# Optimization experiments

Measured on AMD Instinct MI355X. Metric: run time of the kernel, lower is better.

Reference implementation:

```python
import jax, jax.numpy as jnp
import numpy as np

N_NODES = 100_000
N_EDGES = 1_600_000
VOCAB = 128
NUM_GRAPHS = 2048


def setup_inputs() -> dict:
    key = jax.random.key(0)
    ks = jax.random.split(key, 8)
    node_ids = jax.random.randint(ks[0], (N_NODES,), 0, VOCAB)
    edge_index = jax.random.randint(ks[1], (2, N_EDGES), 0, N_NODES)
    batch = jnp.sort(jax.random.randint(ks[2], (N_NODES,), 0, NUM_GRAPHS))
    emb = jax.random.normal(ks[3], (VOCAB, 64), jnp.float32) * 0.1
    W1 = jax.random.normal(ks[4], (64, 128), jnp.float32) * (1.0 / np.sqrt(64))
    b1 = jnp.zeros((128,), jnp.float32)
    W2 = jax.random.normal(ks[5], (128, 64), jnp.float32) * (1.0 / np.sqrt(128))
    b2 = jnp.zeros((64,), jnp.float32)
    fc_w = jax.random.normal(ks[6], (1, 64), jnp.float32) * (1.0 / np.sqrt(64))
    fc_b = jnp.zeros((1,), jnp.float32)
    return {"node_ids": node_ids, "edge_index": edge_index, "batch": batch,
            "emb": emb, "W1": W1, "b1": b1, "W2": W2, "b2": b2,
            "fc_w": fc_w, "fc_b": fc_b}


def _gcn_layer(x, W, b, src, dst, norm, n_nodes):
    # x: [N, Fin] -> transform then gather-normalize-scatter (PyG GCNConv)
    h = x @ W                                   # [N, Fout]
    msg = norm[:, None] * h[src]                # [E+N, Fout]
    out = jax.ops.segment_sum(msg, dst, num_segments=n_nodes)
    return out + b


def reference(node_ids, edge_index, batch, emb, W1, b1, W2, b2, fc_w, fc_b):
    n = node_ids.shape[0]
    loop = jnp.arange(n, dtype=edge_index.dtype)
    src = jnp.concatenate([edge_index[0], loop])    # self-loops added (GCNConv default)
    dst = jnp.concatenate([edge_index[1], loop])
    # symmetric normalization: deg^{-1/2}[src] * deg^{-1/2}[dst], deg from dst (in-degree incl. self-loop)
    deg = jax.ops.segment_sum(jnp.ones_like(src, dtype=jnp.float32), dst, num_segments=n)
    dis = jax.lax.rsqrt(jnp.maximum(deg, 1.0))
    norm = dis[src] * dis[dst]

    x = emb[node_ids]                                # [N, 64]
    x = jax.nn.relu(_gcn_layer(x, W1, b1, src, dst, norm, n))
    x = jax.nn.relu(_gcn_layer(x, W2, b2, src, dst, norm, n))

    # global mean pool over graphs
    counts = jax.ops.segment_sum(jnp.ones((n,), jnp.float32), batch, num_segments=NUM_GRAPHS)
    pooled = jax.ops.segment_sum(x, batch, num_segments=NUM_GRAPHS)
    pooled = pooled / jnp.maximum(counts, 1.0)[:, None]   # [G, 64]
    # dropout is identity in eval mode
    logits = pooled @ fc_w.T + fc_b                 # [G, 1]
    return jax.nn.sigmoid(logits).squeeze(-1)       # [G]
```

## Files before the change

kernel.cpp:

```cpp
#include <hip/hip_runtime.h>
#include <math.h>

typedef short short8 __attribute__((ext_vector_type(8)));
typedef float f32x4 __attribute__((ext_vector_type(4)));

#define WP 132
#define OP 136
#define SC_C 8192
#define SC_NB 832
#define GCAP 1024
#define DG_SUB 16
#define DG_LCAP 1024


__device__ __forceinline__ short f2bf(float x) {
    unsigned u = __float_as_uint(x);
    u += 0x7fffu + ((u >> 16) & 1u);
    return (short)(u >> 16);
}

__global__ void k_cnt(const int* __restrict__ dst, int* __restrict__ wcnt,
                      int E, int N) {
    int lane = threadIdx.x & 63;
    int gw = blockIdx.x * 4 + (threadIdx.x >> 6);
    int TOT = gridDim.x * 4;
    int cnt[8] = {0, 0, 0, 0, 0, 0, 0, 0};
    for (long long base = (long long)gw * 64; base < E; base += (long long)TOT * 64) {
        int i = (int)base + lane;
        bool valid = (i < E);
        int d = valid ? dst[i] : 0;
        int b = valid ? (int)(((long long)d * 8) / N) : -1;
#pragma unroll
        for (int k = 0; k < 8; ++k)
            cnt[k] += (int)__popcll(__ballot(b == k));
    }
#pragma unroll
    for (int k = 0; k < 8; ++k)
        if (lane == 0) wcnt[k * TOT + gw] = cnt[k];
}

__global__ void k_scat(const int* __restrict__ src, const int* __restrict__ dst,
                       const int* __restrict__ wscan, unsigned* __restrict__ sp1,
                       int E, int N) {
    int lane = threadIdx.x & 63;
    int gw = blockIdx.x * 4 + (threadIdx.x >> 6);
    int TOT = gridDim.x * 4;
    int cur[8];
#pragma unroll
    for (int k = 0; k < 8; ++k) cur[k] = wscan[k * TOT + gw];
    for (long long base = (long long)gw * 64; base < E; base += (long long)TOT * 64) {
        int i = (int)base + lane;
        bool valid = (i < E);
        int d = 0, s = 0;
        if (valid) { d = dst[i]; s = src[i]; }
        int b = valid ? (int)(((long long)d * 8) / N) : -1;
        unsigned packed = 0;
        if (valid) {
            int lo = (int)((long long)N * b / 8);
            packed = ((unsigned)s << 14) | (unsigned)(d - lo);
        }
#pragma unroll
        for (int k = 0; k < 8; ++k) {
            unsigned long long mk = __ballot(b == k);
            if (b == k) {
                int pref = (int)__popcll(mk & ((1ull << lane) - 1ull));
                sp1[cur[k] + pref] = packed;
            }
            cur[k] += (int)__popcll(mk);
        }
    }
}

__global__ __launch_bounds__(1024) void k_deg3(
        const unsigned* __restrict__ sp1, const int* __restrict__ wscan,
        int* __restrict__ degi2, int E, int N, int TOTW) {
    __shared__ int h[DG_LCAP];
    int b   = blockIdx.x & 7;
    int hf  = (blockIdx.x >> 3) & 1;
    int sb  = blockIdx.x >> 4;
    int tid = threadIdx.x;
    int lo = (int)((long long)N * b / 8);
    int hi = (int)((long long)N * (b + 1) / 8);
    int range = hi - lo;
    int sub = (range + DG_SUB - 1) / DG_SUB;
    int nlo = sb * sub;
    int nhi = min(nlo + sub, range);
    int cnt = nhi - nlo;
    if (cnt <= 0) return;
    for (int i = tid; i < cnt; i += 1024) h[i] = 0;
    __syncthreads();
    int beg = wscan[b * TOTW];
    int end = (b < 7) ? wscan[(b + 1) * TOTW] : E;
    int span = end - beg;
    int hb = beg + hf * (span >> 1);
    int he = (hf == 0) ? (beg + (span >> 1)) : end;
    for (int i = hb + tid; i < he; i += 1024) {
        int dl = (int)(sp1[i] & 16383u) - nlo;
        if ((unsigned)dl < (unsigned)cnt) atomicAdd(&h[dl], 1);
    }
    __syncthreads();
    int* dout = degi2 + (size_t)hf * N + lo + nlo;
    for (int i = tid; i < cnt; i += 1024) dout[i] = h[i];
}

__global__ void k_tcur(const int* __restrict__ rowptr, int* __restrict__ tcur,
                       int T, int N) {
    int t = blockIdx.x * 256 + threadIdx.x;
    if (t < T) tcur[t] = rowptr[min(16 * t, N)];
}

__global__ __launch_bounds__(256) void k_scat2(
        const unsigned* __restrict__ sp1, const int* __restrict__ wscan,
        int* __restrict__ tcur, unsigned* __restrict__ sp2,
        int E, int N, int TOTW) {
    __shared__ unsigned staged[SC_C];
    __shared__ int hist[SC_NB], hstart[SC_NB], hoff[SC_NB], gbase[SC_NB];
    __shared__ int sdata[256];
    int b = blockIdx.x & 7;
    int nb = gridDim.x >> 3, bi = blockIdx.x >> 3;
    int lo = (int)((long long)N * b / 8);
    int t0 = lo >> 4;
    int beg = wscan[b * TOTW];
    int end = (b < 7) ? wscan[(b + 1) * TOTW] : E;
    int tid = threadIdx.x;

    for (int cb = beg + bi * SC_C; cb < end; cb += nb * SC_C) {
        int count = min(SC_C, end - cb);
        for (int j = tid; j < SC_NB; j += 256) hist[j] = 0;
        __syncthreads();

        unsigned v[SC_C / 256];
#pragma unroll
        for (int j = 0; j < SC_C / 256; ++j) {
            int i = j * 256 + tid;
            v[j] = 0;
            if (i < count) {
                unsigned sp = sp1[cb + i];
                v[j] = sp;
                int d = (int)(sp & 16383u) + lo;
                atomicAdd(&hist[(d >> 4) - t0], 1);
            }
        }
        __syncthreads();

        int loc[4]; int lsum = 0;
#pragma unroll
        for (int j = 0; j < 4; ++j) {
            int idx = tid * 4 + j;
            loc[j] = (idx < SC_NB) ? hist[idx] : 0;
            lsum += loc[j];
        }
        sdata[tid] = lsum;
        __syncthreads();
        for (int off = 1; off < 256; off <<= 1) {
            int add = (tid >= off) ? sdata[tid - off] : 0;
            __syncthreads();
            sdata[tid] += add;
            __syncthreads();
        }
        int excl = sdata[tid] - lsum;
        int run = 0;
#pragma unroll
        for (int j = 0; j < 4; ++j) {
            int idx = tid * 4 + j;
            if (idx < SC_NB) { hstart[idx] = excl + run; hoff[idx] = excl + run; }
            run += loc[j];
        }
        __syncthreads();

        for (int j = tid; j < SC_NB; j += 256)
            if (hist[j] > 0) gbase[j] = atomicAdd(&tcur[t0 + j], hist[j]);
#pragma unroll
        for (int j = 0; j < SC_C / 256; ++j) {
            int i = j * 256 + tid;
            if (i < count) {
                int d = (int)(v[j] & 16383u) + lo;
                int bin = (d >> 4) - t0;
                int old = atomicAdd(&hoff[bin], 1);
                staged[old] = v[j];
            }
        }
        __syncthreads();

        for (int i = tid; i < count; i += 256) {
            unsigned sp = staged[i];
            int d = (int)(sp & 16383u) + lo;
            int bin = (d >> 4) - t0;
            int pos = gbase[bin] + (i - hstart[bin]);
            unsigned s = sp >> 14;
            sp2[pos] = (s << 4) | (unsigned)(d & 15);
        }
        __syncthreads();
    }
}

__global__ void k_scan_a(const int* __restrict__ in, const int* __restrict__ in2,
                         int* __restrict__ outp, int* __restrict__ csums,
                         float* __restrict__ dis, const int* __restrict__ nid,
                         int2* __restrict__ ndpk, int n) {
    __shared__ int sdata[256];
    int tid = threadIdx.x;
    int idx = blockIdx.x * 1024 + tid * 4;
    int v[4];
#pragma unroll
    for (int j = 0; j < 4; ++j) {
        v[j] = 0;
        if (idx + j < n) {
            v[j] = in[idx + j];
            if (in2 != nullptr) v[j] += in2[idx + j];
            if (dis != nullptr) {
                float dv = rsqrtf((float)(v[j] + 1));
                dis[idx + j] = dv;
                int2 nd; nd.x = nid[idx + j]; nd.y = __float_as_int(dv);
                ndpk[idx + j] = nd;
            }
        }
    }
    int tsum = v[0] + v[1] + v[2] + v[3];
    sdata[tid] = tsum;
    __syncthreads();
    for (int off = 1; off < 256; off <<= 1) {
        int add = (tid >= off) ? sdata[tid - off] : 0;
        __syncthreads();
        sdata[tid] += add;
        __syncthreads();
    }
    int excl = sdata[tid] - tsum;
    int run = 0;
#pragma unroll
    for (int j = 0; j < 4; ++j) {
        if (idx + j < n) outp[idx + j] = excl + run;
        run += v[j];
    }
    if (tid == 255) csums[blockIdx.x] = sdata[255];
}

__global__ void k_scan_b(int* __restrict__ csums, int nch) {
    __shared__ int sdata[256];
    int tid = threadIdx.x;
    int v[4];
#pragma unroll
    for (int j = 0; j < 4; ++j) {
        int i = tid * 4 + j;
        v[j] = (i < nch) ? csums[i] : 0;
    }
    int tsum = v[0] + v[1] + v[2] + v[3];
    sdata[tid] = tsum;
    __syncthreads();
    for (int off = 1; off < 256; off <<= 1) {
        int add = (tid >= off) ? sdata[tid - off] : 0;
        __syncthreads();
        sdata[tid] += add;
        __syncthreads();
    }
    int excl = sdata[tid] - tsum;
    int run = 0;
#pragma unroll
    for (int j = 0; j < 4; ++j) {
        int i = tid * 4 + j;
        if (i < nch) csums[i] = excl + run;
        run += v[j];
    }
}

__global__ void k_scan_c(int* __restrict__ outp, const int* __restrict__ csums,
                         int n, int E, int writeTail) {
    int idx = blockIdx.x * 1024 + threadIdx.x * 4;
    int add = csums[blockIdx.x];
#pragma unroll
    for (int j = 0; j < 4; ++j)
        if (idx + j < n) outp[idx + j] += add;
    if (writeTail && blockIdx.x == 0 && threadIdx.x == 0) outp[n] = E;
}

__global__ void k_tabs(const float* __restrict__ emb, const float* __restrict__ W1,
                       const float* __restrict__ W2,
                       short* __restrict__ T1T, short* __restrict__ W2T) {
    int id = blockIdx.x * 256 + threadIdx.x;
    if (id < 128 * 128) {
        int f = id >> 7, c = id & 127;
        float acc = 0.f;
#pragma unroll
        for (int k = 0; k < 64; ++k) acc += emb[c * 64 + k] * W1[k * 128 + f];
        T1T[id] = f2bf(acc);
    } else {
        int id2 = id - 128 * 128;
        if (id2 < 64 * 128) {
            int f = id2 >> 7, k = id2 & 127;
            W2T[id2] = f2bf(W2[k * 64 + f]);
        }
    }
}

__global__ __launch_bounds__(256) void k_fused(
        const int* __restrict__ rowptr, const unsigned* __restrict__ sp2,
        const int2* __restrict__ ndpk, const float* __restrict__ dis,
        const short* __restrict__ T1T, const short* __restrict__ W2T,
        const float* __restrict__ b1, unsigned short* __restrict__ g, int N) {
    __shared__ float wtile[16 * WP];
    __shared__ unsigned short otile[16 * OP];
    int tid = threadIdx.x;
    int v0 = blockIdx.x * 16;
    int nloc = min(16, N - v0);

    for (int i = tid; i < 16 * WP; i += 256) wtile[i] = 0.f;
    __syncthreads();

    if (tid < nloc) {
        int2 nd = ndpk[v0 + tid];
        atomicAdd(&wtile[tid * WP + nd.x], __int_as_float(nd.y));
    }
    int e0 = rowptr[v0], e1 = rowptr[min(v0 + 16, N)];
    for (int base = e0; base < e1; base += 1024) {
        unsigned sp[4];
        int2 nd[4];
#pragma unroll
        for (int j = 0; j < 4; ++j) {
            int i = base + tid + j * 256;
            sp[j] = (i < e1) ? sp2[i] : 0xffffffffu;
        }
#pragma unroll
        for (int j = 0; j < 4; ++j)
            if (sp[j] != 0xffffffffu) nd[j] = ndpk[sp[j] >> 4];
#pragma unroll
        for (int j = 0; j < 4; ++j)
            if (sp[j] != 0xffffffffu)
                atomicAdd(&wtile[(sp[j] & 15u) * WP + nd[j].x],
                          __int_as_float(nd[j].y));
    }
    __syncthreads();

    int wid = tid >> 6, lane = tid & 63;
    int m = lane & 15, g4 = lane >> 4;

    short8 a[4];
#pragma unroll
    for (int s = 0; s < 4; ++s) {
        float av[8];
        *(f32x4*)(av)     = *(const f32x4*)&wtile[m * WP + g4 * 8 + s * 32];
        *(f32x4*)(av + 4) = *(const f32x4*)&wtile[m * WP + g4 * 8 + s * 32 + 4];
        short8 f;
#pragma unroll
        for (int i = 0; i < 8; ++i) f[i] = f2bf(av[i]);
        a[s] = f;
    }
    float dvals[4];
#pragma unroll
    for (int r = 0; r < 4; ++r) {
        int v = v0 + g4 * 4 + r;
        dvals[r] = (v < N) ? dis[v] : 0.f;
    }

#pragma unroll
    for (int t = 0; t < 2; ++t) {
        int nt = wid * 2 + t;
        f32x4 acc = {0.f, 0.f, 0.f, 0.f};
        const short8* bp = (const short8*)(T1T + (size_t)(nt * 16 + m) * 128 + g4 * 8);
#pragma unroll
        for (int s = 0; s < 4; ++s)
            acc = __builtin_amdgcn_mfma_f32_16x16x32_bf16(a[s], bp[s * 4], acc, 0, 0, 0);
        int col = nt * 16 + m;
        float bb = b1[col];
#pragma unroll
        for (int r = 0; r < 4; ++r) {
            int row = g4 * 4 + r;
            otile[row * OP + col] =
                (unsigned short)f2bf(fmaxf(dvals[r] * acc[r] + bb, 0.f));
        }
    }
    __syncthreads();

    short8 a2[4];
#pragma unroll
    for (int s = 0; s < 4; ++s)
        a2[s] = *(const short8*)&otile[m * OP + g4 * 8 + s * 32];
    {
        int nt2 = wid;
        f32x4 acc = {0.f, 0.f, 0.f, 0.f};
        const short8* bp = (const short8*)(W2T + (size_t)(nt2 * 16 + m) * 128 + g4 * 8);
#pragma unroll
        for (int s = 0; s < 4; ++s)
            acc = __builtin_amdgcn_mfma_f32_16x16x32_bf16(a2[s], bp[s * 4], acc, 0, 0, 0);
#pragma unroll
        for (int r = 0; r < 4; ++r) {
            int row = g4 * 4 + r;
            if (row < nloc)
                g[(size_t)(v0 + row) * 64 + nt2 * 16 + m] =
                    (unsigned short)f2bf(dvals[r] * acc[r]);
        }
    }
}

__global__ __launch_bounds__(256) void k_gather3(
        const unsigned* __restrict__ sp2, const int* __restrict__ rowptr,
        const unsigned short* __restrict__ g, const float* __restrict__ dis,
        const float* __restrict__ b2, float* __restrict__ x, int N) {
    __shared__ int lbuf[GCAP];
    __shared__ int lrp[17];
    __shared__ int ncur[16];
    int tid = threadIdx.x;
    int v0 = blockIdx.x * 16;
    int nloc = min(16, N - v0);
    if (tid < 17) lrp[tid] = rowptr[min(v0 + tid, N)];
    __syncthreads();
    int e0 = lrp[0], e1 = lrp[nloc];
    int span = e1 - e0;
    bool fits = (span <= GCAP);

    if (fits) {
        if (tid < 16) ncur[tid] = lrp[tid] - e0;
        __syncthreads();
        for (int i = e0 + tid; i < e1; i += 256) {
            unsigned sp = sp2[i];
            int old = atomicAdd(&ncur[sp & 15u], 1);
            lbuf[old] = (int)(sp >> 4);
        }
        __syncthreads();
    }

    int q = tid >> 4, l = tid & 15;
    if (q >= nloc) return;
    int v = v0 + q;
    const uint2* g64 = (const uint2*)g;

    uint2 su = g64[(size_t)v * 16 + l];
    f32x4 acc;
    acc[0] = __uint_as_float(su.x << 16);
    acc[1] = __uint_as_float(su.x & 0xffff0000u);
    acc[2] = __uint_as_float(su.y << 16);
    acc[3] = __uint_as_float(su.y & 0xffff0000u);

    if (fits) {
        int e = lrp[q] - e0, re = lrp[q + 1] - e0;
        while (e < re) {
            int cnt = re - e;
            uint2 u[8];
#pragma unroll
            for (int j = 0; j < 8; ++j) {
                int s = lbuf[min(e + j, re - 1)];
                u[j] = g64[(size_t)s * 16 + l];
            }
#pragma unroll
            for (int j = 0; j < 8; ++j) {
                float mask = (j < cnt) ? 1.f : 0.f;
                acc[0] += mask * __uint_as_float(u[j].x << 16);
                acc[1] += mask * __uint_as_float(u[j].x & 0xffff0000u);
                acc[2] += mask * __uint_as_float(u[j].y << 16);
                acc[3] += mask * __uint_as_float(u[j].y & 0xffff0000u);
            }
            e += 8;
        }
    } else {
        for (int i = e0; i < e1; ++i) {
            unsigned sp = sp2[i];
            if ((int)(sp & 15u) == q) {
                int s = (int)(sp >> 4);
                uint2 u = g64[(size_t)s * 16 + l];
                acc[0] += __uint_as_float(u.x << 16);
                acc[1] += __uint_as_float(u.x & 0xffff0000u);
                acc[2] += __uint_as_float(u.y << 16);
                acc[3] += __uint_as_float(u.y & 0xffff0000u);
            }
        }
    }
    float dv = dis[v];
    f32x4 bb = *(const f32x4*)(b2 + l * 4);
    f32x4 r;
#pragma unroll
    for (int j = 0; j < 4; ++j) r[j] = fmaxf(dv * acc[j] + bb[j], 0.f);
    *(f32x4*)(x + (size_t)v * 64 + l * 4) = r;
}

__global__ void k_bounds(const int* __restrict__ batch, int* __restrict__ gstart,
                         int* __restrict__ gend, int n) {
    int i = blockIdx.x * 256 + threadIdx.x;
    if (i >= n) return;
    int b = batch[i];
    if (i == 0 || batch[i - 1] != b) gstart[b] = i;
    if (i == n - 1 || batch[i + 1] != b) gend[b] = i + 1;
}

__global__ __launch_bounds__(256) void k_pool2(
        const float* __restrict__ x, const int* __restrict__ gstart,
        const int* __restrict__ gend, const float* __restrict__ fc_w,
        const float* __restrict__ fc_b, float* __restrict__ out) {
    __shared__ float red[4][64];
    int gi = blockIdx.x;
    int tid = threadIdx.x, wid = tid >> 6, lane = tid & 63;
    int s = gstart[gi], epos = gend[gi];
    float acc = 0.f;
    for (int r = s + wid; r < epos; r += 4) acc += x[(size_t)r * 64 + lane];
    red[wid][lane] = acc;
    __syncthreads();
    if (wid == 0) {
        float a = red[0][lane] + red[1][lane] + red[2][lane] + red[3][lane];
        float cnt = fmaxf((float)(epos - s), 1.0f);
        a = (a / cnt) * fc_w[lane];
#pragma unroll
        for (int off = 32; off >= 1; off >>= 1) a += __shfl_down(a, off);
        if (lane == 0) out[gi] = 1.0f / (1.0f + expf(-(a + fc_b[0])));
    }
}

extern "C" void kernel_launch(void* const* d_in, const int* in_sizes, int n_in,
                              void* d_out, int out_size, void* d_ws, size_t ws_size,
                              hipStream_t stream) {
    const int*   nid   = (const int*)d_in[0];
    const int*   eidx  = (const int*)d_in[1];
    const int*   batch = (const int*)d_in[2];
    const float* emb   = (const float*)d_in[3];
    const float* W1    = (const float*)d_in[4];
    const float* b1    = (const float*)d_in[5];
    const float* W2    = (const float*)d_in[6];
    const float* b2    = (const float*)d_in[7];
    const float* fcw   = (const float*)d_in[8];
    const float* fcb   = (const float*)d_in[9];

    const int N = in_sizes[0];
    const int E = in_sizes[1] / 2;
    const int G = out_size;
    const int T = (N + 15) / 16;
    const int* src = eidx;
    const int* dst = eidx + E;

    char* p = (char*)d_ws;
    auto alloc = [&](size_t bytes) {
        char* r = p;
        p += (bytes + 255) & ~(size_t)255;
        return r;
    };
    const int PBLK = 2048;
    const int TOTW = PBLK * 4;
    const int NW   = 8 * TOTW;
    int*      degi2  = (int*)     alloc((size_t)N * 2 * 4);
    float*    dis    = (float*)   alloc((size_t)N * 4);
    int2*     ndpk   = (int2*)    alloc((size_t)N * 8);
    short*    T1T    = (short*)   alloc(128 * 128 * 2);
    short*    W2T    = (short*)   alloc(64 * 128 * 2);
    int*      rowptr = (int*)     alloc((size_t)(N + 1) * 4);
    int*      csums  = (int*)     alloc(4096 * 4);
    int*      wcnt   = (int*)     alloc((size_t)NW * 4);
    int*      wscan  = (int*)     alloc((size_t)(NW + 1) * 4);
    int*      csums2 = (int*)     alloc(256 * 4);
    int*      tcur   = (int*)     alloc((size_t)(T + 1) * 4);
    unsigned* sp1    = (unsigned*)alloc((size_t)E * 4);
    unsigned* sp2    = (unsigned*)alloc((size_t)E * 4);
    unsigned short* g = (unsigned short*)alloc((size_t)N * 64 * 2);
    float*    x      = (float*)   alloc((size_t)N * 64 * 4);
    int*      gstart = (int*)     alloc((size_t)G * 4);
    int*      gend   = (int*)     alloc((size_t)G * 4);

    hipMemsetAsync(gstart, 0, (size_t)G * 4, stream);
    hipMemsetAsync(gend, 0, (size_t)G * 4, stream);

    k_cnt<<<PBLK, 256, 0, stream>>>(dst, wcnt, E, N);

    int nch2 = (NW + 1023) / 1024;
    k_scan_a<<<nch2, 256, 0, stream>>>(wcnt, nullptr, wscan, csums2,
                                       nullptr, nullptr, nullptr, NW);
    k_scan_b<<<1, 256, 0, stream>>>(csums2, nch2);
    k_scan_c<<<nch2, 256, 0, stream>>>(wscan, csums2, NW, 0, 0);

    k_scat<<<PBLK, 256, 0, stream>>>(src, dst, wscan, sp1, E, N);
    k_deg3<<<8 * DG_SUB * 2, 1024, 0, stream>>>(sp1, wscan, degi2, E, N, TOTW);

    int nch = (N + 1023) / 1024;
    k_scan_a<<<nch, 256, 0, stream>>>(degi2, degi2 + N, rowptr, csums,
                                      dis, nid, ndpk, N);
    k_scan_b<<<1, 256, 0, stream>>>(csums, nch);
    k_scan_c<<<nch, 256, 0, stream>>>(rowptr, csums, N, E, 1);

    k_tcur<<<(T + 255) / 256, 256, 0, stream>>>(rowptr, tcur, T, N);
    k_scat2<<<2048, 256, 0, stream>>>(sp1, wscan, tcur, sp2, E, N, TOTW);

    k_tabs<<<96, 256, 0, stream>>>(emb, W1, W2, T1T, W2T);

    k_fused<<<T, 256, 0, stream>>>(rowptr, sp2, ndpk, dis, T1T, W2T, b1, g, N);

    k_gather3<<<T, 256, 0, stream>>>(sp2, rowptr, g, dis, b2, x, N);

    k_bounds<<<(N + 255) / 256, 256, 0, stream>>>(batch, gstart, gend, N);
    k_pool2<<<G, 256, 0, stream>>>(x, gstart, gend, fcw, fcb, (float*)d_out);
}
```

Before: 177.3 us.

## Fold tile-cursor init into scan and widen fused layer tile to 32 nodes

New measurement: 177.9 us (median of 5 runs). No clear change (+0.4%).

```diff
diff --git a/kernel.cpp b/kernel.cpp
--- a/kernel.cpp
+++ b/kernel.cpp
@@ -103,12 +103,6 @@
     for (int i = tid; i < cnt; i += 1024) dout[i] = h[i];
 }
 
-__global__ void k_tcur(const int* __restrict__ rowptr, int* __restrict__ tcur,
-                       int T, int N) {
-    int t = blockIdx.x * 256 + threadIdx.x;
-    if (t < T) tcur[t] = rowptr[min(16 * t, N)];
-}
-
 __global__ __launch_bounds__(256) void k_scat2(
         const unsigned* __restrict__ sp1, const int* __restrict__ wscan,
         int* __restrict__ tcur, unsigned* __restrict__ sp2,
@@ -264,12 +258,18 @@
 }
 
 __global__ void k_scan_c(int* __restrict__ outp, const int* __restrict__ csums,
-                         int n, int E, int writeTail) {
+                         int n, int E, int writeTail, int* __restrict__ tcur) {
     int idx = blockIdx.x * 1024 + threadIdx.x * 4;
     int add = csums[blockIdx.x];
 #pragma unroll
-    for (int j = 0; j < 4; ++j)
-        if (idx + j < n) outp[idx + j] += add;
+    for (int j = 0; j < 4; ++j) {
+        int k = idx + j;
+        if (k < n) {
+            int r = outp[k] + add;
+            outp[k] = r;
+            if (tcur != nullptr && (k & 15) == 0) tcur[k >> 4] = r;
+        }
+    }
     if (writeTail && blockIdx.x == 0 && threadIdx.x == 0) outp[n] = E;
 }
 
@@ -297,27 +297,30 @@
         const int2* __restrict__ ndpk, const float* __restrict__ dis,
         const short* __restrict__ T1T, const short* __restrict__ W2T,
         const float* __restrict__ b1, unsigned short* __restrict__ g, int N) {
-    __shared__ float wtile[16 * WP];
-    __shared__ unsigned short otile[16 * OP];
+    __shared__ float wtile[32 * WP];
+    __shared__ unsigned short otile[32 * OP];
     int tid = threadIdx.x;
-    int v0 = blockIdx.x * 16;
-    int nloc = min(16, N - v0);
-
-    for (int i = tid; i < 16 * WP; i += 256) wtile[i] = 0.f;
+    int v0 = blockIdx.x * 32;
+    int nloc = min(32, N - v0);
+
+    for (int i = tid; i < 32 * WP; i += 256) wtile[i] = 0.f;
     __syncthreads();
 
     if (tid < nloc) {
         int2 nd = ndpk[v0 + tid];
         atomicAdd(&wtile[tid * WP + nd.x], __int_as_float(nd.y));
     }
-    int e0 = rowptr[v0], e1 = rowptr[min(v0 + 16, N)];
+    int e0   = rowptr[v0];
+    int emid = (nloc > 16) ? rowptr[v0 + 16] : rowptr[v0 + nloc];
+    int e1   = rowptr[min(v0 + 32, N)];
     for (int base = e0; base < e1; base += 1024) {
-        unsigned sp[4];
-        int2 nd[4];
+        unsigned sp[4]; int hi16[4]; int2 nd[4];
 #pragma unroll
         for (int j = 0; j < 4; ++j) {
             int i = base + tid + j * 256;
-            sp[j] = (i < e1) ? sp2[i] : 0xffffffffu;
+            bool ok = (i < e1);
+            sp[j] = ok ? sp2[i] : 0xffffffffu;
+            hi16[j] = (ok && i >= emid) ? 16 : 0;
         }
 #pragma unroll
         for (int j = 0; j < 4; ++j)
@@ -325,20 +328,23 @@
 #pragma unroll
         for (int j = 0; j < 4; ++j)
             if (sp[j] != 0xffffffffu)
-                atomicAdd(&wtile[(sp[j] & 15u) * WP + nd[j].x],
+                atomicAdd(&wtile[((sp[j] & 15u) + hi16[j]) * WP + nd[j].x],
                           __int_as_float(nd[j].y));
     }
     __syncthreads();
 
     int wid = tid >> 6, lane = tid & 63;
     int m = lane & 15, g4 = lane >> 4;
+    int rh = wid >> 1;
+    int cg = wid & 1;
 
     short8 a[4];
 #pragma unroll
     for (int s = 0; s < 4; ++s) {
         float av[8];
-        *(f32x4*)(av)     = *(const f32x4*)&wtile[m * WP + g4 * 8 + s * 32];
-        *(f32x4*)(av + 4) = *(const f32x4*)&wtile[m * WP + g4 * 8 + s * 32 + 4];
+        int row = rh * 16 + m;
+        *(f32x4*)(av)     = *(const f32x4*)&wtile[row * WP + g4 * 8 + s * 32];
+        *(f32x4*)(av + 4) = *(const f32x4*)&wtile[row * WP + g4 * 8 + s * 32 + 4];
         short8 f;
 #pragma unroll
         for (int i = 0; i < 8; ++i) f[i] = f2bf(av[i]);
@@ -347,13 +353,13 @@
     float dvals[4];
 #pragma unroll
     for (int r = 0; r < 4; ++r) {
-        int v = v0 + g4 * 4 + r;
+        int v = v0 + rh * 16 + g4 * 4 + r;
         dvals[r] = (v < N) ? dis[v] : 0.f;
     }
 
 #pragma unroll
-    for (int t = 0; t < 2; ++t) {
-        int nt = wid * 2 + t;
+    for (int t = 0; t < 4; ++t) {
+        int nt = cg * 4 + t;
         f32x4 acc = {0.f, 0.f, 0.f, 0.f};
         const short8* bp = (const short8*)(T1T + (size_t)(nt * 16 + m) * 128 + g4 * 8);
 #pragma unroll
@@ -363,7 +369,7 @@
         float bb = b1[col];
 #pragma unroll
         for (int r = 0; r < 4; ++r) {
-            int row = g4 * 4 + r;
+            int row = rh * 16 + g4 * 4 + r;
             otile[row * OP + col] =
                 (unsigned short)f2bf(fmaxf(dvals[r] * acc[r] + bb, 0.f));
         }
@@ -373,9 +379,10 @@
     short8 a2[4];
 #pragma unroll
     for (int s = 0; s < 4; ++s)
-        a2[s] = *(const short8*)&otile[m * OP + g4 * 8 + s * 32];
-    {
-        int nt2 = wid;
+        a2[s] = *(const short8*)&otile[(rh * 16 + m) * OP + g4 * 8 + s * 32];
+#pragma unroll
+    for (int t = 0; t < 2; ++t) {
+        int nt2 = cg * 2 + t;
         f32x4 acc = {0.f, 0.f, 0.f, 0.f};
         const short8* bp = (const short8*)(W2T + (size_t)(nt2 * 16 + m) * 128 + g4 * 8);
 #pragma unroll
@@ -383,7 +390,7 @@
             acc = __builtin_amdgcn_mfma_f32_16x16x32_bf16(a2[s], bp[s * 4], acc, 0, 0, 0);
 #pragma unroll
         for (int r = 0; r < 4; ++r) {
-            int row = g4 * 4 + r;
+            int row = rh * 16 + g4 * 4 + r;
             if (row < nloc)
                 g[(size_t)(v0 + row) * 64 + nt2 * 16 + m] =
                     (unsigned short)f2bf(dvals[r] * acc[r]);
@@ -559,7 +566,7 @@
     k_scan_a<<<nch2, 256, 0, stream>>>(wcnt, nullptr, wscan, csums2,
                                        nullptr, nullptr, nullptr, NW);
     k_scan_b<<<1, 256, 0, stream>>>(csums2, nch2);
-    k_scan_c<<<nch2, 256, 0, stream>>>(wscan, csums2, NW, 0, 0);
+    k_scan_c<<<nch2, 256, 0, stream>>>(wscan, csums2, NW, 0, 0, nullptr);
 
     k_scat<<<PBLK, 256, 0, stream>>>(src, dst, wscan, sp1, E, N);
     k_deg3<<<8 * DG_SUB * 2, 1024, 0, stream>>>(sp1, wscan, degi2, E, N, TOTW);
@@ -568,14 +575,14 @@
     k_scan_a<<<nch, 256, 0, stream>>>(degi2, degi2 + N, rowptr, csums,
                                       dis, nid, ndpk, N);
     k_scan_b<<<1, 256, 0, stream>>>(csums, nch);
-    k_scan_c<<<nch, 256, 0, stream>>>(rowptr, csums, N, E, 1);
-
-    k_tcur<<<(T + 255) / 256, 256, 0, stream>>>(rowptr, tcur, T, N);
+    k_scan_c<<<nch, 256, 0, stream>>>(rowptr, csums, N, E, 1, tcur);
+
     k_scat2<<<2048, 256, 0, stream>>>(sp1, wscan, tcur, sp2, E, N, TOTW);
 
     k_tabs<<<96, 256, 0, stream>>>(emb, W1, W2, T1T, W2T);
 
-    k_fused<<<T, 256, 0, stream>>>(rowptr, sp2, ndpk, dis, T1T, W2T, b1, g, N);
+    k_fused<<<(N + 31) / 32, 256, 0, stream>>>(rowptr, sp2, ndpk, dis, T1T, W2T,
+                                               b1, g, N);
 
     k_gather3<<<T, 256, 0, stream>>>(sp2, rowptr, g, dis, b2, x, N);
 
```

## Pack source node id and dis into sp2 during scatter, fold tcur into scan

Applied to the files above, without the earlier changes.

After: 181.4 us. 1.02x slower.

```diff
diff --git a/kernel.cpp b/kernel.cpp
--- a/kernel.cpp
+++ b/kernel.cpp
@@ -103,16 +103,10 @@
     for (int i = tid; i < cnt; i += 1024) dout[i] = h[i];
 }
 
-__global__ void k_tcur(const int* __restrict__ rowptr, int* __restrict__ tcur,
-                       int T, int N) {
-    int t = blockIdx.x * 256 + threadIdx.x;
-    if (t < T) tcur[t] = rowptr[min(16 * t, N)];
-}
-
 __global__ __launch_bounds__(256) void k_scat2(
         const unsigned* __restrict__ sp1, const int* __restrict__ wscan,
-        int* __restrict__ tcur, unsigned* __restrict__ sp2,
-        int E, int N, int TOTW) {
+        int* __restrict__ tcur, int2* __restrict__ sp2,
+        const int2* __restrict__ ndpk, int E, int N, int TOTW) {
     __shared__ unsigned staged[SC_C];
     __shared__ int hist[SC_NB], hstart[SC_NB], hoff[SC_NB], gbase[SC_NB];
     __shared__ int sdata[256];
@@ -182,13 +176,30 @@
         }
         __syncthreads();
 
-        for (int i = tid; i < count; i += 256) {
-            unsigned sp = staged[i];
-            int d = (int)(sp & 16383u) + lo;
-            int bin = (d >> 4) - t0;
-            int pos = gbase[bin] + (i - hstart[bin]);
-            unsigned s = sp >> 14;
-            sp2[pos] = (s << 4) | (unsigned)(d & 15);
+        for (int i = tid; i < count; i += 1024) {
+            unsigned spl[4];
+#pragma unroll
+            for (int j = 0; j < 4; ++j) {
+                int k2 = i + j * 256;
+                spl[j] = (k2 < count) ? staged[k2] : 0xffffffffu;
+            }
+            int2 ndv[4];
+#pragma unroll
+            for (int j = 0; j < 4; ++j)
+                if (spl[j] != 0xffffffffu) ndv[j] = ndpk[spl[j] >> 14];
+#pragma unroll
+            for (int j = 0; j < 4; ++j) {
+                if (spl[j] == 0xffffffffu) continue;
+                int k2 = i + j * 256;
+                int d = (int)(spl[j] & 16383u) + lo;
+                int bin = (d >> 4) - t0;
+                int pos = gbase[bin] + (k2 - hstart[bin]);
+                int2 outv;
+                outv.x = (int)(((spl[j] >> 14) << 4) | (unsigned)(d & 15));
+                outv.y = (int)(((unsigned)ndv[j].x << 25) |
+                               ((unsigned)ndv[j].y >> 7));
+                sp2[pos] = outv;
+            }
         }
         __syncthreads();
     }
@@ -264,12 +275,18 @@
 }
 
 __global__ void k_scan_c(int* __restrict__ outp, const int* __restrict__ csums,
-                         int n, int E, int writeTail) {
+                         int n, int E, int writeTail, int* __restrict__ tcur) {
     int idx = blockIdx.x * 1024 + threadIdx.x * 4;
     int add = csums[blockIdx.x];
 #pragma unroll
-    for (int j = 0; j < 4; ++j)
-        if (idx + j < n) outp[idx + j] += add;
+    for (int j = 0; j < 4; ++j) {
+        int k = idx + j;
+        if (k < n) {
+            int r = outp[k] + add;
+            outp[k] = r;
+            if (tcur != nullptr && (k & 15) == 0) tcur[k >> 4] = r;
+        }
+    }
     if (writeTail && blockIdx.x == 0 && threadIdx.x == 0) outp[n] = E;
 }
 
@@ -293,7 +310,7 @@
 }
 
 __global__ __launch_bounds__(256) void k_fused(
-        const int* __restrict__ rowptr, const unsigned* __restrict__ sp2,
+        const int* __restrict__ rowptr, const int2* __restrict__ sp2,
         const int2* __restrict__ ndpk, const float* __restrict__ dis,
         const short* __restrict__ T1T, const short* __restrict__ W2T,
         const float* __restrict__ b1, unsigned short* __restrict__ g, int N) {
@@ -311,22 +328,12 @@
         atomicAdd(&wtile[tid * WP + nd.x], __int_as_float(nd.y));
     }
     int e0 = rowptr[v0], e1 = rowptr[min(v0 + 16, N)];
-    for (int base = e0; base < e1; base += 1024) {
-        unsigned sp[4];
-        int2 nd[4];
-#pragma unroll
-        for (int j = 0; j < 4; ++j) {
-            int i = base + tid + j * 256;
-            sp[j] = (i < e1) ? sp2[i] : 0xffffffffu;
-        }
-#pragma unroll
-        for (int j = 0; j < 4; ++j)
-            if (sp[j] != 0xffffffffu) nd[j] = ndpk[sp[j] >> 4];
-#pragma unroll
-        for (int j = 0; j < 4; ++j)
-            if (sp[j] != 0xffffffffu)
-                atomicAdd(&wtile[(sp[j] & 15u) * WP + nd[j].x],
-                          __int_as_float(nd[j].y));
+    for (int i = e0 + tid; i < e1; i += 256) {
+        int2 ev = sp2[i];
+        int dl = ev.x & 15;
+        int c = (int)((unsigned)ev.y >> 25);
+        float dv = __uint_as_float(((unsigned)ev.y & 0x01ffffffu) << 7);
+        atomicAdd(&wtile[dl * WP + c], dv);
     }
     __syncthreads();
 
@@ -392,7 +399,7 @@
 }
 
 __global__ __launch_bounds__(256) void k_gather3(
-        const unsigned* __restrict__ sp2, const int* __restrict__ rowptr,
+        const int2* __restrict__ sp2, const int* __restrict__ rowptr,
         const unsigned short* __restrict__ g, const float* __restrict__ dis,
         const float* __restrict__ b2, float* __restrict__ x, int N) {
     __shared__ int lbuf[GCAP];
@@ -411,7 +418,7 @@
         if (tid < 16) ncur[tid] = lrp[tid] - e0;
         __syncthreads();
         for (int i = e0 + tid; i < e1; i += 256) {
-            unsigned sp = sp2[i];
+            unsigned sp = (unsigned)sp2[i].x;
             int old = atomicAdd(&ncur[sp & 15u], 1);
             lbuf[old] = (int)(sp >> 4);
         }
@@ -452,7 +459,7 @@
         }
     } else {
         for (int i = e0; i < e1; ++i) {
-            unsigned sp = sp2[i];
+            unsigned sp = (unsigned)sp2[i].x;
             if ((int)(sp & 15u) == q) {
                 int s = (int)(sp >> 4);
                 uint2 u = g64[(size_t)s * 16 + l];
@@ -544,7 +551,7 @@
     int*      csums2 = (int*)     alloc(256 * 4);
     int*      tcur   = (int*)     alloc((size_t)(T + 1) * 4);
     unsigned* sp1    = (unsigned*)alloc((size_t)E * 4);
-    unsigned* sp2    = (unsigned*)alloc((size_t)E * 4);
+    int2*     sp2    = (int2*)    alloc((size_t)E * 8);
     unsigned short* g = (unsigned short*)alloc((size_t)N * 64 * 2);
     float*    x      = (float*)   alloc((size_t)N * 64 * 4);
     int*      gstart = (int*)     alloc((size_t)G * 4);
@@ -559,7 +566,7 @@
     k_scan_a<<<nch2, 256, 0, stream>>>(wcnt, nullptr, wscan, csums2,
                                        nullptr, nullptr, nullptr, NW);
     k_scan_b<<<1, 256, 0, stream>>>(csums2, nch2);
-    k_scan_c<<<nch2, 256, 0, stream>>>(wscan, csums2, NW, 0, 0);
+    k_scan_c<<<nch2, 256, 0, stream>>>(wscan, csums2, NW, 0, 0, nullptr);
 
     k_scat<<<PBLK, 256, 0, stream>>>(src, dst, wscan, sp1, E, N);
     k_deg3<<<8 * DG_SUB * 2, 1024, 0, stream>>>(sp1, wscan, degi2, E, N, TOTW);
@@ -568,10 +575,9 @@
     k_scan_a<<<nch, 256, 0, stream>>>(degi2, degi2 + N, rowptr, csums,
                                       dis, nid, ndpk, N);
     k_scan_b<<<1, 256, 0, stream>>>(csums, nch);
-    k_scan_c<<<nch, 256, 0, stream>>>(rowptr, csums, N, E, 1);
-
-    k_tcur<<<(T + 255) / 256, 256, 0, stream>>>(rowptr, tcur, T, N);
-    k_scat2<<<2048, 256, 0, stream>>>(sp1, wscan, tcur, sp2, E, N, TOTW);
+    k_scan_c<<<nch, 256, 0, stream>>>(rowptr, csums, N, E, 1, tcur);
+
+    k_scat2<<<2048, 256, 0, stream>>>(sp1, wscan, tcur, sp2, ndpk, E, N, TOTW);
 
     k_tabs<<<96, 256, 0, stream>>>(emb, W1, W2, T1T, W2T);
 
```

## Fuse mean-pool into layer-2 gather and merge small setup kernels

Applied to the files above, without the earlier changes.

Result: faster. 169.8 us (-4.2%).

```diff
diff --git a/kernel.cpp b/kernel.cpp
--- a/kernel.cpp
+++ b/kernel.cpp
@@ -19,11 +19,32 @@
     return (short)(u >> 16);
 }
 
-__global__ void k_cnt(const int* __restrict__ dst, int* __restrict__ wcnt,
-                      int E, int N) {
+__global__ void k_cnt_tabs(const int* __restrict__ dst, int* __restrict__ wcnt,
+                           const float* __restrict__ emb,
+                           const float* __restrict__ W1,
+                           const float* __restrict__ W2,
+                           short* __restrict__ T1T, short* __restrict__ W2T,
+                           int E, int N, int PBLK) {
+    if (blockIdx.x >= PBLK) {
+        int id = (blockIdx.x - PBLK) * 256 + threadIdx.x;
+        if (id < 128 * 128) {
+            int f = id >> 7, c = id & 127;
+            float acc = 0.f;
+#pragma unroll
+            for (int k = 0; k < 64; ++k) acc += emb[c * 64 + k] * W1[k * 128 + f];
+            T1T[id] = f2bf(acc);
+        } else {
+            int id2 = id - 128 * 128;
+            if (id2 < 64 * 128) {
+                int f = id2 >> 7, k = id2 & 127;
+                W2T[id2] = f2bf(W2[k * 64 + f]);
+            }
+        }
+        return;
+    }
     int lane = threadIdx.x & 63;
     int gw = blockIdx.x * 4 + (threadIdx.x >> 6);
-    int TOT = gridDim.x * 4;
+    int TOT = PBLK * 4;
     int cnt[8] = {0, 0, 0, 0, 0, 0, 0, 0};
     for (long long base = (long long)gw * 64; base < E; base += (long long)TOT * 64) {
         int i = (int)base + lane;
@@ -103,12 +124,6 @@
     for (int i = tid; i < cnt; i += 1024) dout[i] = h[i];
 }
 
-__global__ void k_tcur(const int* __restrict__ rowptr, int* __restrict__ tcur,
-                       int T, int N) {
-    int t = blockIdx.x * 256 + threadIdx.x;
-    if (t < T) tcur[t] = rowptr[min(16 * t, N)];
-}
-
 __global__ __launch_bounds__(256) void k_scat2(
         const unsigned* __restrict__ sp1, const int* __restrict__ wscan,
         int* __restrict__ tcur, unsigned* __restrict__ sp2,
@@ -264,32 +279,19 @@
 }
 
 __global__ void k_scan_c(int* __restrict__ outp, const int* __restrict__ csums,
-                         int n, int E, int writeTail) {
+                         int n, int E, int writeTail, int* __restrict__ tcur) {
     int idx = blockIdx.x * 1024 + threadIdx.x * 4;
     int add = csums[blockIdx.x];
 #pragma unroll
-    for (int j = 0; j < 4; ++j)
-        if (idx + j < n) outp[idx + j] += add;
+    for (int j = 0; j < 4; ++j) {
+        int k = idx + j;
+        if (k < n) {
+            int r = outp[k] + add;
+            outp[k] = r;
+            if (tcur != nullptr && (k & 15) == 0) tcur[k >> 4] = r;
+        }
+    }
     if (writeTail && blockIdx.x == 0 && threadIdx.x == 0) outp[n] = E;
-}
-
-__global__ void k_tabs(const float* __restrict__ emb, const float* __restrict__ W1,
-                       const float* __restrict__ W2,
-                       short* __restrict__ T1T, short* __restrict__ W2T) {
-    int id = blockIdx.x * 256 + threadIdx.x;
-    if (id < 128 * 128) {
-        int f = id >> 7, c = id & 127;
-        float acc = 0.f;
-#pragma unroll
-        for (int k = 0; k < 64; ++k) acc += emb[c * 64 + k] * W1[k * 128 + f];
-        T1T[id] = f2bf(acc);
-    } else {
-        int id2 = id - 128 * 128;
-        if (id2 < 64 * 128) {
-            int f = id2 >> 7, k = id2 & 127;
-            W2T[id2] = f2bf(W2[k * 64 + f]);
-        }
-    }
 }
 
 __global__ __launch_bounds__(256) void k_fused(
@@ -394,14 +396,21 @@
 __global__ __launch_bounds__(256) void k_gather3(
         const unsigned* __restrict__ sp2, const int* __restrict__ rowptr,
         const unsigned short* __restrict__ g, const float* __restrict__ dis,
-        const float* __restrict__ b2, float* __restrict__ x, int N) {
+        const float* __restrict__ b2, const int* __restrict__ batch,
+        float* __restrict__ pooled, int N) {
     __shared__ int lbuf[GCAP];
     __shared__ int lrp[17];
     __shared__ int ncur[16];
+    __shared__ int sb[16];
+    __shared__ float xt[16][64];
     int tid = threadIdx.x;
     int v0 = blockIdx.x * 16;
     int nloc = min(16, N - v0);
     if (tid < 17) lrp[tid] = rowptr[min(v0 + tid, N)];
+    if (tid >= 32 && tid < 48) {
+        int r = tid - 32;
+        sb[r] = batch[min(v0 + r, N - 1)];
+    }
     __syncthreads();
     int e0 = lrp[0], e1 = lrp[nloc];
     int span = e1 - e0;
@@ -419,87 +428,96 @@
     }
 
     int q = tid >> 4, l = tid & 15;
-    if (q >= nloc) return;
-    int v = v0 + q;
-    const uint2* g64 = (const uint2*)g;
-
-    uint2 su = g64[(size_t)v * 16 + l];
-    f32x4 acc;
-    acc[0] = __uint_as_float(su.x << 16);
-    acc[1] = __uint_as_float(su.x & 0xffff0000u);
-    acc[2] = __uint_as_float(su.y << 16);
-    acc[3] = __uint_as_float(su.y & 0xffff0000u);
-
-    if (fits) {
-        int e = lrp[q] - e0, re = lrp[q + 1] - e0;
-        while (e < re) {
-            int cnt = re - e;
-            uint2 u[8];
-#pragma unroll
-            for (int j = 0; j < 8; ++j) {
-                int s = lbuf[min(e + j, re - 1)];
-                u[j] = g64[(size_t)s * 16 + l];
-            }
-#pragma unroll
-            for (int j = 0; j < 8; ++j) {
-                float mask = (j < cnt) ? 1.f : 0.f;
-                acc[0] += mask * __uint_as_float(u[j].x << 16);
-                acc[1] += mask * __uint_as_float(u[j].x & 0xffff0000u);
-                acc[2] += mask * __uint_as_float(u[j].y << 16);
-                acc[3] += mask * __uint_as_float(u[j].y & 0xffff0000u);
-            }
-            e += 8;
-        }
-    } else {
-        for (int i = e0; i < e1; ++i) {
-            unsigned sp = sp2[i];
-            if ((int)(sp & 15u) == q) {
-                int s = (int)(sp >> 4);
-                uint2 u = g64[(size_t)s * 16 + l];
-                acc[0] += __uint_as_float(u.x << 16);
-                acc[1] += __uint_as_float(u.x & 0xffff0000u);
-                acc[2] += __uint_as_float(u.y << 16);
-                acc[3] += __uint_as_float(u.y & 0xffff0000u);
-            }
-        }
-    }
-    float dv = dis[v];
-    f32x4 bb = *(const f32x4*)(b2 + l * 4);
-    f32x4 r;
-#pragma unroll
-    for (int j = 0; j < 4; ++j) r[j] = fmaxf(dv * acc[j] + bb[j], 0.f);
-    *(f32x4*)(x + (size_t)v * 64 + l * 4) = r;
-}
-
-__global__ void k_bounds(const int* __restrict__ batch, int* __restrict__ gstart,
-                         int* __restrict__ gend, int n) {
-    int i = blockIdx.x * 256 + threadIdx.x;
-    if (i >= n) return;
-    int b = batch[i];
-    if (i == 0 || batch[i - 1] != b) gstart[b] = i;
-    if (i == n - 1 || batch[i + 1] != b) gend[b] = i + 1;
-}
-
-__global__ __launch_bounds__(256) void k_pool2(
-        const float* __restrict__ x, const int* __restrict__ gstart,
-        const int* __restrict__ gend, const float* __restrict__ fc_w,
-        const float* __restrict__ fc_b, float* __restrict__ out) {
-    __shared__ float red[4][64];
-    int gi = blockIdx.x;
-    int tid = threadIdx.x, wid = tid >> 6, lane = tid & 63;
-    int s = gstart[gi], epos = gend[gi];
-    float acc = 0.f;
-    for (int r = s + wid; r < epos; r += 4) acc += x[(size_t)r * 64 + lane];
-    red[wid][lane] = acc;
-    __syncthreads();
-    if (wid == 0) {
-        float a = red[0][lane] + red[1][lane] + red[2][lane] + red[3][lane];
-        float cnt = fmaxf((float)(epos - s), 1.0f);
-        a = (a / cnt) * fc_w[lane];
-#pragma unroll
-        for (int off = 32; off >= 1; off >>= 1) a += __shfl_down(a, off);
-        if (lane == 0) out[gi] = 1.0f / (1.0f + expf(-(a + fc_b[0])));
-    }
+    if (q < nloc) {
+        int v = v0 + q;
+        const uint2* g64 = (const uint2*)g;
+
+        uint2 su = g64[(size_t)v * 16 + l];
+        f32x4 acc;
+        acc[0] = __uint_as_float(su.x << 16);
+        acc[1] = __uint_as_float(su.x & 0xffff0000u);
+        acc[2] = __uint_as_float(su.y << 16);
+        acc[3] = __uint_as_float(su.y & 0xffff0000u);
+
+        if (fits) {
+            int e = lrp[q] - e0, re = lrp[q + 1] - e0;
+            while (e < re) {
+                int cnt = re - e;
+                uint2 u[8];
+#pragma unroll
+                for (int j = 0; j < 8; ++j) {
+                    int s = lbuf[min(e + j, re - 1)];
+                    u[j] = g64[(size_t)s * 16 + l];
+                }
+#pragma unroll
+                for (int j = 0; j < 8; ++j) {
+                    float mask = (j < cnt) ? 1.f : 0.f;
+                    acc[0] += mask * __uint_as_float(u[j].x << 16);
+                    acc[1] += mask * __uint_as_float(u[j].x & 0xffff0000u);
+                    acc[2] += mask * __uint_as_float(u[j].y << 16);
+                    acc[3] += mask * __uint_as_float(u[j].y & 0xffff0000u);
+                }
+                e += 8;
+            }
+        } else {
+            for (int i = e0; i < e1; ++i) {
+                unsigned sp = sp2[i];
+                if ((int)(sp & 15u) == q) {
+                    int s = (int)(sp >> 4);
+                    uint2 u = g64[(size_t)s * 16 + l];
+                    acc[0] += __uint_as_float(u.x << 16);
+                    acc[1] += __uint_as_float(u.x & 0xffff0000u);
+                    acc[2] += __uint_as_float(u.y << 16);
+                    acc[3] += __uint_as_float(u.y & 0xffff0000u);
+                }
+            }
+        }
+        float dv = dis[v];
+        f32x4 bb = *(const f32x4*)(b2 + l * 4);
+#pragma unroll
+        for (int j = 0; j < 4; ++j)
+            xt[q][l * 4 + j] = fmaxf(dv * acc[j] + bb[j], 0.f);
+    }
+    __syncthreads();
+
+    if (tid < 64) {
+        float acc = 0.f;
+        int bprev = sb[0];
+        for (int r = 0; r < nloc; ++r) {
+            int b = sb[r];
+            if (b != bprev) {
+                atomicAdd(&pooled[(size_t)bprev * 64 + tid], acc);
+                acc = 0.f;
+                bprev = b;
+            }
+            acc += xt[r][tid];
+        }
+        atomicAdd(&pooled[(size_t)bprev * 64 + tid], acc);
+    }
+}
+
+__device__ __forceinline__ int lower_bound(const int* __restrict__ a, int n, int key) {
+    int lo = 0, hi = n;
+    while (lo < hi) {
+        int mid = (lo + hi) >> 1;
+        if (a[mid] < key) lo = mid + 1; else hi = mid;
+    }
+    return lo;
+}
+
+__global__ void k_head(const float* __restrict__ pooled, const int* __restrict__ batch,
+                       const float* __restrict__ fc_w, const float* __restrict__ fc_b,
+                       float* __restrict__ out, int N, int ngraphs) {
+    int gi = (blockIdx.x * 256 + threadIdx.x) >> 6;
+    int lane = threadIdx.x & 63;
+    if (gi >= ngraphs) return;
+    int s = lower_bound(batch, N, gi);
+    int e = lower_bound(batch, N, gi + 1);
+    float c = fmaxf((float)(e - s), 1.0f);
+    float a = (pooled[(size_t)gi * 64 + lane] / c) * fc_w[lane];
+#pragma unroll
+    for (int off = 32; off >= 1; off >>= 1) a += __shfl_down(a, off);
+    if (lane == 0) out[gi] = 1.0f / (1.0f + expf(-(a + fc_b[0])));
 }
 
 extern "C" void kernel_launch(void* const* d_in, const int* in_sizes, int n_in,
@@ -546,20 +564,18 @@
     unsigned* sp1    = (unsigned*)alloc((size_t)E * 4);
     unsigned* sp2    = (unsigned*)alloc((size_t)E * 4);
     unsigned short* g = (unsigned short*)alloc((size_t)N * 64 * 2);
-    float*    x      = (float*)   alloc((size_t)N * 64 * 4);
-    int*      gstart = (int*)     alloc((size_t)G * 4);
-    int*      gend   = (int*)     alloc((size_t)G * 4);
-
-    hipMemsetAsync(gstart, 0, (size_t)G * 4, stream);
-    hipMemsetAsync(gend, 0, (size_t)G * 4, stream);
-
-    k_cnt<<<PBLK, 256, 0, stream>>>(dst, wcnt, E, N);
+    float*    pooled = (float*)   alloc((size_t)G * 64 * 4);
+
+    hipMemsetAsync(pooled, 0, (size_t)G * 64 * 4, stream);
+
+    k_cnt_tabs<<<PBLK + 96, 256, 0, stream>>>(dst, wcnt, emb, W1, W2, T1T, W2T,
+                                              E, N, PBLK);
 
     int nch2 = (NW + 1023) / 1024;
     k_scan_a<<<nch2, 256, 0, stream>>>(wcnt, nullptr, wscan, csums2,
                                        nullptr, nullptr, nullptr, NW);
     k_scan_b<<<1, 256, 0, stream>>>(csums2, nch2);
-    k_scan_c<<<nch2, 256, 0, stream>>>(wscan, csums2, NW, 0, 0);
+    k_scan_c<<<nch2, 256, 0, stream>>>(wscan, csums2, NW, 0, 0, nullptr);
 
     k_scat<<<PBLK, 256, 0, stream>>>(src, dst, wscan, sp1, E, N);
     k_deg3<<<8 * DG_SUB * 2, 1024, 0, stream>>>(sp1, wscan, degi2, E, N, TOTW);
@@ -568,17 +584,14 @@
     k_scan_a<<<nch, 256, 0, stream>>>(degi2, degi2 + N, rowptr, csums,
                                       dis, nid, ndpk, N);
     k_scan_b<<<1, 256, 0, stream>>>(csums, nch);
-    k_scan_c<<<nch, 256, 0, stream>>>(rowptr, csums, N, E, 1);
-
-    k_tcur<<<(T + 255) / 256, 256, 0, stream>>>(rowptr, tcur, T, N);
+    k_scan_c<<<nch, 256, 0, stream>>>(rowptr, csums, N, E, 1, tcur);
+
     k_scat2<<<2048, 256, 0, stream>>>(sp1, wscan, tcur, sp2, E, N, TOTW);
 
-    k_tabs<<<96, 256, 0, stream>>>(emb, W1, W2, T1T, W2T);
-
     k_fused<<<T, 256, 0, stream>>>(rowptr, sp2, ndpk, dis, T1T, W2T, b1, g, N);
 
-    k_gather3<<<T, 256, 0, stream>>>(sp2, rowptr, g, dis, b2, x, N);
-
-    k_bounds<<<(N + 255) / 256, 256, 0, stream>>>(batch, gstart, gend, N);
-    k_pool2<<<G, 256, 0, stream>>>(x, gstart, gend, fcw, fcb, (float*)d_out);
-}
+    k_gather3<<<T, 256, 0, stream>>>(sp2, rowptr, g, dis, b2, batch, pooled, N);
+
+    k_head<<<((long long)G * 64 + 255) / 256, 256, 0, stream>>>(
+        pooled, batch, fcw, fcb, (float*)d_out, N, G);
+}
```
